# Performance work log

Hardware: AMD Instinct MI355X
Metric: run time of the kernel (lower is better)

The kernel has to match this reference:

```python
import jax, jax.numpy as jnp
import numpy as np

LOSS_WEIGHT = 0.01
CONF_THRESH = 0.8
B, N, D = 2, 12288, 256
N_CLUSTERS = 64


def setup_inputs() -> dict:
    key = jax.random.key(0)
    k1, k2, k3, k4 = jax.random.split(key, 4)
    # Clustered features so that pseudo-label confidences exceed the 0.8 threshold
    # (pure iid randn would give max cosine sim ~0.25 and a degenerate zero loss).
    centers = jax.random.normal(k1, (N_CLUSTERS, D), dtype=jnp.float32)
    ids = jax.random.randint(k2, (B, N), 0, N_CLUSTERS)
    feat_3d = centers[ids] + 0.1 * jax.random.normal(k3, (B, N, D), dtype=jnp.float32)
    valid_mask = jax.random.randint(k4, (B, N), 0, 2) == 1
    return {"feat_3d": feat_3d, "valid_mask": valid_mask}


def reference(feat_3d, valid_mask):
    # F.normalize: x / max(||x||, eps), eps=1e-12
    eps = 1e-12
    norm = jnp.sqrt(jnp.sum(feat_3d * feat_3d, axis=-1, keepdims=True))
    nf = feat_3d / jnp.maximum(norm, eps)                      # [B, N, D]

    # Full cosine-similarity matrix per scene; invalid columns masked to -inf-like.
    sim = jnp.einsum('bnd,bmd->bnm', nf, nf)                   # [B, N, N]
    neg = jnp.finfo(sim.dtype).min
    sim = jnp.where(valid_mask[:, None, :], sim, neg)
    max_sim = jnp.max(sim, axis=-1)                            # [B, N] row-max over valid cols

    invalid = ~valid_mask
    has_valid = jnp.any(valid_mask, axis=-1)                   # [B]
    has_invalid = jnp.any(invalid, axis=-1)                    # [B]

    # Only rows that are invalid points, with max similarity over valid points > threshold.
    confident = invalid & (max_sim > CONF_THRESH) & has_valid[:, None]
    n_conf = jnp.sum(confident, axis=-1)                       # [B]
    n_inv = jnp.sum(invalid, axis=-1).astype(jnp.float32)      # [B]

    contrib = jnp.where(confident, 1.0 - max_sim, 0.0)
    pseudo = jnp.sum(contrib, axis=-1) / jnp.maximum(n_conf, 1).astype(jnp.float32)

    # Scene is skipped if no valid / no invalid points or zero confident matches.
    active = (n_conf > 0) & has_valid & has_invalid
    total_loss = jnp.sum(jnp.where(active, pseudo * n_inv, 0.0))
    total_pts = jnp.sum(jnp.where(active, n_inv, 0.0))
    return jnp.where(total_pts > 0, LOSS_WEIGHT * total_loss / total_pts, 0.0)
```

## Files before the change

### kernel.cpp

```cpp
#include <hip/hip_runtime.h>

#define NTOT 12288
#define DIM  256
#define NB   2
#define BROWS 512
#define CGRP  256
#define NT    4
#define TILEB 32768
#define NGC   32
#define NRB   16

typedef __attribute__((ext_vector_type(8))) _Float16 f16x8;
typedef __attribute__((ext_vector_type(16))) float f32x16;

__device__ __forceinline__ unsigned toOrd(float f) {
    unsigned u = __float_as_uint(f);
    return (u & 0x80000000u) ? ~u : (u | 0x80000000u);
}
__device__ __forceinline__ float fromOrd(unsigned u) {
    unsigned b = (u & 0x80000000u) ? (u ^ 0x80000000u) : ~u;
    return __uint_as_float(b);
}
__device__ __forceinline__ void load_lds16(const void* g, void* l) {
    __builtin_amdgcn_global_load_lds(
        (const __attribute__((address_space(1))) unsigned int*)g,
        (__attribute__((address_space(3))) unsigned int*)l, 16, 0, 0);
}


__global__ __launch_bounds__(1024) void k_scan(
    const int* __restrict__ mask, int* __restrict__ inv,
    unsigned* __restrict__ maxsim, int* __restrict__ cnts)
{
    int b = blockIdx.x;
    int tid = threadIdx.x;
    int lane = tid & 63, w = tid >> 6;
    __shared__ int wsum[16];

    int mv[12];
    #pragma unroll
    for (int j = 0; j < 12; j++) mv[j] = mask[b * NTOT + j * 1024 + tid] ? 1 : 0;

    int running = 0;
    #pragma unroll
    for (int j = 0; j < 12; j++) {
        int i = j * 1024 + tid;
        int m = mv[j];
        int v = m;
        #pragma unroll
        for (int off = 1; off < 64; off <<= 1) {
            int t = __shfl_up(v, off);
            if (lane >= off) v += t;
        }
        if (lane == 63) wsum[w] = v;
        __syncthreads();
        int woff = 0, ctot = 0;
        #pragma unroll
        for (int k = 0; k < 16; k++) { int s = wsum[k]; ctot += s; if (k < w) woff += s; }
        int ex = running + woff + v - m;
        int d = m ? ex : (NTOT - 1 - (i - ex));
        inv[b * NTOT + d] = i;
        maxsim[b * NTOT + i] = 0u;
        running += ctot;
        __syncthreads();
    }
    if (tid == 0) { cnts[b] = running; cnts[NB + b] = NTOT - running; }
}

__global__ __launch_bounds__(256) void k_norm(
    const float* __restrict__ feat, const int* __restrict__ inv, ushort* __restrict__ pk)
{
    int blk = blockIdx.x;
    int b = blk / (NTOT / 32);
    int panel = blk % (NTOT / 32);
    int tid = threadIdx.x;
    int r = tid >> 3, c = tid & 7;
    int d = panel * 32 + r;
    int i = inv[b * NTOT + d];
    const float* src = feat + ((size_t)b * NTOT + i) * DIM + c * 32;

    float x[32]; float ss = 0.f;
    #pragma unroll
    for (int j = 0; j < 8; j++) {
        float4 v = *(const float4*)(src + j * 4);
        x[j*4+0] = v.x; x[j*4+1] = v.y; x[j*4+2] = v.z; x[j*4+3] = v.w;
        ss += v.x*v.x + v.y*v.y + v.z*v.z + v.w*v.w;
    }
    ss += __shfl_xor(ss, 1); ss += __shfl_xor(ss, 2); ss += __shfl_xor(ss, 4);
    float invn = 1.0f / fmaxf(sqrtf(ss), 1e-12f);

    ushort* pbout = pk + (size_t)b * NTOT * DIM;
    #pragma unroll
    for (int g = 0; g < 4; g++) {
        f16x8 hv;
        #pragma unroll
        for (int e = 0; e < 8; e++) hv[e] = (_Float16)(x[g*8+e] * invn);
        int kc = c * 2 + (g >> 1), kh = g & 1;
        *(f16x8*)(pbout + (size_t)(panel * 16 + kc) * 512 + (kh * 32 + r) * 8) = hv;
    }
}

__global__ __launch_bounds__(512, 2) void k_gemm(
    const ushort* __restrict__ pk, unsigned* __restrict__ maxsim, const int* __restrict__ cnts)
{
    int b = blockIdx.z;
    int nval = cnts[b];
    int ninv = cnts[NB + b];
    int bx = blockIdx.x;
    int by = blockIdx.y;
    if (bx * CGRP >= nval || by * BROWS >= ninv) return;
    int rowA0 = NTOT - (by + 1) * BROWS;
    int colG0 = bx * CGRP;
    int pA0 = rowA0 >> 5, pBg = colG0 >> 5;

    __shared__ __align__(16) char smem[4 * TILEB];

    int tid = threadIdx.x, lane = tid & 63, w = tid >> 6;
    const ushort* pb = pk + (size_t)b * NTOT * DIM;

    f16x8 a[2][16];
    {
        const ushort* abase = pb + (size_t)(pA0 + w * 2) * 16 * 512 + lane * 8;
        #pragma unroll
        for (int mt = 0; mt < 2; mt++)
            #pragma unroll
            for (int ks = 0; ks < 16; ks++)
                a[mt][ks] = *(const f16x8*)(abase + (size_t)(mt * 16 + ks) * 512);
    }
    __builtin_amdgcn_sched_barrier(0);

#define STAGE(t) { const int bo_ = ((t) & 3) * TILEB; const int p0_ = pBg + (t) * 2;     \
    _Pragma("unroll")                                                                    \
    for (int c_ = 0; c_ < 4; c_++) {                                                     \
        int c__ = w * 4 + c_;                                                            \
        const ushort* g__ = pb + ((size_t)(p0_ + (c__ >> 4)) * 16 + (c__ & 15)) * 512 + lane * 8; \
        load_lds16(g__, smem + bo_ + c__ * 1024);                                        \
    }                                                                                    \
    __builtin_amdgcn_sched_barrier(0); }

    STAGE(0); STAGE(1); STAGE(2);

    float mrow[2][16];
    #pragma unroll
    for (int mt = 0; mt < 2; mt++)
        #pragma unroll
        for (int rr = 0; rr < 16; rr++) mrow[mt][rr] = -INFINITY;

    const f32x16 zacc = {};

    #pragma unroll
    for (int t = 0; t < NT; t++) {
        if (t <= 1)      asm volatile("s_waitcnt vmcnt(8)" ::: "memory");
        else if (t == 2) asm volatile("s_waitcnt vmcnt(4)" ::: "memory");
        else             asm volatile("s_waitcnt vmcnt(0)" ::: "memory");
        __builtin_amdgcn_s_barrier();
        __builtin_amdgcn_sched_barrier(0);
        if (t + 3 < NT) STAGE(t + 3);

        const char* sb = smem + (t & 3) * TILEB;
        #pragma unroll
        for (int nt = 0; nt < 2; nt++) {
            f32x16 acc[2] = {zacc, zacc};
            #pragma unroll
            for (int kq = 0; kq < 4; kq++) {
                f16x8 bg[4];
                #pragma unroll
                for (int k4 = 0; k4 < 4; k4++)
                    bg[k4] = *(const f16x8*)(sb + (nt * 16 + kq * 4 + k4) * 1024 + lane * 16);
                #pragma unroll
                for (int k4 = 0; k4 < 4; k4++)
                    #pragma unroll
                    for (int mt = 0; mt < 2; mt++)
                        acc[mt] = __builtin_amdgcn_mfma_f32_32x32x16_f16(
                            a[mt][kq * 4 + k4], bg[k4], acc[mt], 0, 0, 0);
            }
            int cg = colG0 + t * 64 + nt * 32 + (lane & 31);
            bool cv = cg < nval;
            #pragma unroll
            for (int mt = 0; mt < 2; mt++)
                #pragma unroll
                for (int rr = 0; rr < 16; rr++) {
                    float vv = cv ? acc[mt][rr] : -INFINITY;
                    mrow[mt][rr] = fmaxf(mrow[mt][rr], vv);
                }
        }
    }
#undef STAGE

    #pragma unroll
    for (int off = 1; off <= 16; off <<= 1)
        #pragma unroll
        for (int mt = 0; mt < 2; mt++)
            #pragma unroll
            for (int rr = 0; rr < 16; rr++)
                mrow[mt][rr] = fmaxf(mrow[mt][rr], __shfl_xor(mrow[mt][rr], off));

    int cl = lane & 31, hh = lane >> 5;
    if (cl == 0) {
        #pragma unroll
        for (int mt = 0; mt < 2; mt++)
            #pragma unroll
            for (int rr = 0; rr < 16; rr++) {
                int rowg = rowA0 + w * 64 + mt * 32 + (rr & 3) + 8 * (rr >> 2) + 4 * hh;
                atomicMax(maxsim + (size_t)b * NTOT + rowg, toOrd(mrow[mt][rr]));
            }
    }
}

__global__ __launch_bounds__(256) void k_final(
    const unsigned* __restrict__ maxsim, const int* __restrict__ cnts, float* __restrict__ out)
{
    __shared__ float ssum[NB];
    __shared__ int   scnt[NB];
    int tid = threadIdx.x;
    if (tid < NB) { ssum[tid] = 0.0f; scnt[tid] = 0; }
    __syncthreads();

    for (int b = 0; b < NB; b++) {
        int ninv = cnts[NB + b];
        float ls = 0.0f; int lc = 0;
        for (int i = tid; i < ninv; i += 256) {
            int r = NTOT - ninv + i;
            float ms = fromOrd(maxsim[(size_t)b * NTOT + r]);
            if (ms > 0.8f) { ls += 1.0f - ms; lc++; }
        }
        #pragma unroll
        for (int off = 32; off; off >>= 1) {
            ls += __shfl_xor(ls, off);
            lc += __shfl_xor(lc, off);
        }
        if ((tid & 63) == 0) { atomicAdd(&ssum[b], ls); atomicAdd(&scnt[b], lc); }
    }
    __syncthreads();

    if (tid == 0) {
        float tl = 0.0f, tp = 0.0f;
        for (int b = 0; b < NB; b++) {
            int nval = cnts[b], ninv = cnts[NB + b], nc = scnt[b];
            bool active = (nc > 0) && (nval > 0) && (ninv > 0);
            if (active) {
                float pseudo = ssum[b] / (float)(nc > 0 ? nc : 1);
                tl += pseudo * (float)ninv;
                tp += (float)ninv;
            }
        }
        out[0] = (tp > 0.0f) ? (0.01f * tl / tp) : 0.0f;
    }
}

extern "C" void kernel_launch(void* const* d_in, const int* in_sizes, int n_in,
                              void* d_out, int out_size, void* d_ws, size_t ws_size,
                              hipStream_t stream)
{
    const float* feat = (const float*)d_in[0];
    const int*   mask = (const int*)d_in[1];

    char* ws = (char*)d_ws;
    int*      cnts   = (int*)ws;
    int*      inv    = (int*)(ws + 64);
    unsigned* maxsim = (unsigned*)(ws + 98368);
    ushort*   pk     = (ushort*)(ws + 262144);

    hipLaunchKernelGGL(k_scan, dim3(NB), dim3(1024), 0, stream, mask, inv, maxsim, cnts);
    hipLaunchKernelGGL(k_norm, dim3(NB * (NTOT / 32)), dim3(256), 0, stream, feat, inv, pk);
    hipLaunchKernelGGL(k_gemm, dim3(NGC, NRB, NB), dim3(512), 0, stream, pk, maxsim, cnts);
    hipLaunchKernelGGL(k_final, dim3(1), dim3(256), 0, stream, maxsim, cnts, (float*)d_out);
}
```

Before: 159.3 us.

## Split GEMM block work across 16 waves with one M-tile per wave

Doubles the GEMM block to 1024 threads. Each wave now holds a single 32-row A tile instead of two, which halves the A registers and accumulators per wave and lets more waves be resident. Cooperative LDS staging is spread over twice as many waves, the vmcnt waits are adjusted to match, and s_setprio is placed around the MFMA bursts. The final reduction also uses 1024 threads. The trade-off is less MFMA work per B fragment read from LDS, so LDS read traffic per FLOP doubles.

```diff
diff --git a/kernel.cpp b/kernel.cpp
--- a/kernel.cpp
+++ b/kernel.cpp
@@ -100,7 +100,7 @@
     }
 }
 
-__global__ __launch_bounds__(512, 2) void k_gemm(
+__global__ __launch_bounds__(1024, 4) void k_gemm(
     const ushort* __restrict__ pk, unsigned* __restrict__ maxsim, const int* __restrict__ cnts)
 {
     int b = blockIdx.z;
@@ -118,21 +118,19 @@
     int tid = threadIdx.x, lane = tid & 63, w = tid >> 6;
     const ushort* pb = pk + (size_t)b * NTOT * DIM;
 
-    f16x8 a[2][16];
+    f16x8 a[16];
     {
-        const ushort* abase = pb + (size_t)(pA0 + w * 2) * 16 * 512 + lane * 8;
-        #pragma unroll
-        for (int mt = 0; mt < 2; mt++)
-            #pragma unroll
-            for (int ks = 0; ks < 16; ks++)
-                a[mt][ks] = *(const f16x8*)(abase + (size_t)(mt * 16 + ks) * 512);
+        const ushort* abase = pb + (size_t)(pA0 + w) * 16 * 512 + lane * 8;
+        #pragma unroll
+        for (int ks = 0; ks < 16; ks++)
+            a[ks] = *(const f16x8*)(abase + (size_t)ks * 512);
     }
     __builtin_amdgcn_sched_barrier(0);
 
 #define STAGE(t) { const int bo_ = ((t) & 3) * TILEB; const int p0_ = pBg + (t) * 2;     \
     _Pragma("unroll")                                                                    \
-    for (int c_ = 0; c_ < 4; c_++) {                                                     \
-        int c__ = w * 4 + c_;                                                            \
+    for (int c_ = 0; c_ < 2; c_++) {                                                     \
+        int c__ = w * 2 + c_;                                                            \
         const ushort* g__ = pb + ((size_t)(p0_ + (c__ >> 4)) * 16 + (c__ & 15)) * 512 + lane * 8; \
         load_lds16(g__, smem + bo_ + c__ * 1024);                                        \
     }                                                                                    \
@@ -140,18 +138,16 @@
 
     STAGE(0); STAGE(1); STAGE(2);
 
-    float mrow[2][16];
-    #pragma unroll
-    for (int mt = 0; mt < 2; mt++)
-        #pragma unroll
-        for (int rr = 0; rr < 16; rr++) mrow[mt][rr] = -INFINITY;
+    float mrow[16];
+    #pragma unroll
+    for (int rr = 0; rr < 16; rr++) mrow[rr] = -INFINITY;
 
     const f32x16 zacc = {};
 
     #pragma unroll
     for (int t = 0; t < NT; t++) {
-        if (t <= 1)      asm volatile("s_waitcnt vmcnt(8)" ::: "memory");
-        else if (t == 2) asm volatile("s_waitcnt vmcnt(4)" ::: "memory");
+        if (t <= 1)      asm volatile("s_waitcnt vmcnt(4)" ::: "memory");
+        else if (t == 2) asm volatile("s_waitcnt vmcnt(2)" ::: "memory");
         else             asm volatile("s_waitcnt vmcnt(0)" ::: "memory");
         __builtin_amdgcn_s_barrier();
         __builtin_amdgcn_sched_barrier(0);
@@ -160,29 +156,27 @@
         const char* sb = smem + (t & 3) * TILEB;
         #pragma unroll
         for (int nt = 0; nt < 2; nt++) {
-            f32x16 acc[2] = {zacc, zacc};
+            f32x16 acc = zacc;
             #pragma unroll
             for (int kq = 0; kq < 4; kq++) {
                 f16x8 bg[4];
                 #pragma unroll
                 for (int k4 = 0; k4 < 4; k4++)
                     bg[k4] = *(const f16x8*)(sb + (nt * 16 + kq * 4 + k4) * 1024 + lane * 16);
+                __builtin_amdgcn_s_setprio(1);
                 #pragma unroll
                 for (int k4 = 0; k4 < 4; k4++)
-                    #pragma unroll
-                    for (int mt = 0; mt < 2; mt++)
-                        acc[mt] = __builtin_amdgcn_mfma_f32_32x32x16_f16(
-                            a[mt][kq * 4 + k4], bg[k4], acc[mt], 0, 0, 0);
+                    acc = __builtin_amdgcn_mfma_f32_32x32x16_f16(
+                        a[kq * 4 + k4], bg[k4], acc, 0, 0, 0);
+                __builtin_amdgcn_s_setprio(0);
             }
             int cg = colG0 + t * 64 + nt * 32 + (lane & 31);
             bool cv = cg < nval;
             #pragma unroll
-            for (int mt = 0; mt < 2; mt++)
-                #pragma unroll
-                for (int rr = 0; rr < 16; rr++) {
-                    float vv = cv ? acc[mt][rr] : -INFINITY;
-                    mrow[mt][rr] = fmaxf(mrow[mt][rr], vv);
-                }
+            for (int rr = 0; rr < 16; rr++) {
+                float vv = cv ? acc[rr] : -INFINITY;
+                mrow[rr] = fmaxf(mrow[rr], vv);
+            }
         }
     }
 #undef STAGE
@@ -190,24 +184,20 @@
     #pragma unroll
     for (int off = 1; off <= 16; off <<= 1)
         #pragma unroll
-        for (int mt = 0; mt < 2; mt++)
-            #pragma unroll
-            for (int rr = 0; rr < 16; rr++)
-                mrow[mt][rr] = fmaxf(mrow[mt][rr], __shfl_xor(mrow[mt][rr], off));
+        for (int rr = 0; rr < 16; rr++)
+            mrow[rr] = fmaxf(mrow[rr], __shfl_xor(mrow[rr], off));
 
     int cl = lane & 31, hh = lane >> 5;
     if (cl == 0) {
         #pragma unroll
-        for (int mt = 0; mt < 2; mt++)
-            #pragma unroll
-            for (int rr = 0; rr < 16; rr++) {
-                int rowg = rowA0 + w * 64 + mt * 32 + (rr & 3) + 8 * (rr >> 2) + 4 * hh;
-                atomicMax(maxsim + (size_t)b * NTOT + rowg, toOrd(mrow[mt][rr]));
-            }
-    }
-}
-
-__global__ __launch_bounds__(256) void k_final(
+        for (int rr = 0; rr < 16; rr++) {
+            int rowg = rowA0 + w * 32 + (rr & 3) + 8 * (rr >> 2) + 4 * hh;
+            atomicMax(maxsim + (size_t)b * NTOT + rowg, toOrd(mrow[rr]));
+        }
+    }
+}
+
+__global__ __launch_bounds__(1024) void k_final(
     const unsigned* __restrict__ maxsim, const int* __restrict__ cnts, float* __restrict__ out)
 {
     __shared__ float ssum[NB];
@@ -219,7 +209,7 @@
     for (int b = 0; b < NB; b++) {
         int ninv = cnts[NB + b];
         float ls = 0.0f; int lc = 0;
-        for (int i = tid; i < ninv; i += 256) {
+        for (int i = tid; i < ninv; i += 1024) {
             int r = NTOT - ninv + i;
             float ms = fromOrd(maxsim[(size_t)b * NTOT + r]);
             if (ms > 0.8f) { ls += 1.0f - ms; lc++; }
@@ -263,6 +253,6 @@
 
     hipLaunchKernelGGL(k_scan, dim3(NB), dim3(1024), 0, stream, mask, inv, maxsim, cnts);
     hipLaunchKernelGGL(k_norm, dim3(NB * (NTOT / 32)), dim3(256), 0, stream, feat, inv, pk);
-    hipLaunchKernelGGL(k_gemm, dim3(NGC, NRB, NB), dim3(512), 0, stream, pk, maxsim, cnts);
-    hipLaunchKernelGGL(k_final, dim3(1), dim3(256), 0, stream, maxsim, cnts, (float*)d_out);
-}
+    hipLaunchKernelGGL(k_gemm, dim3(NGC, NRB, NB), dim3(1024), 0, stream, pk, maxsim, cnts);
+    hipLaunchKernelGGL(k_final, dim3(1), dim3(1024), 0, stream, maxsim, cnts, (float*)d_out);
+}
```

Result: no change. 158.3 us (-0.6%).

## Fuse final reduction into GEMM via last-block counter and retile GEMM grid

Applied to the files above, without the earlier changes.

Removes the separate k_final launch: each GEMM block bumps a global counter after its atomics, and the last block to finish runs the loss reduction. The GEMM moves to 256-thread blocks with 256-row tiles, a 26x26 grid sized to cover the valid and invalid halves more tightly, double buffering instead of four stages, and s_setprio around the MFMA bursts. k_norm now stages each packed panel in LDS so the global writes are coalesced. The risks are more blocks with less A-reuse per block, and a grid-wide counter whose correctness relies on the fence ordering.

```diff
diff --git a/kernel.cpp b/kernel.cpp
--- a/kernel.cpp
+++ b/kernel.cpp
@@ -3,12 +3,13 @@
 #define NTOT 12288
 #define DIM  256
 #define NB   2
-#define BROWS 512
+#define BROWS 256
 #define CGRP  256
 #define NT    4
 #define TILEB 32768
-#define NGC   32
-#define NRB   16
+#define NGC   26
+#define NRB   26
+#define GRID_TOT (NGC * NRB * NB)
 
 typedef __attribute__((ext_vector_type(8))) _Float16 f16x8;
 typedef __attribute__((ext_vector_type(16))) float f32x16;
@@ -36,6 +37,8 @@
     int tid = threadIdx.x;
     int lane = tid & 63, w = tid >> 6;
     __shared__ int wsum[16];
+
+    if (b == 0 && tid == 0) ((unsigned*)cnts)[4] = 0u;
 
     int mv[12];
     #pragma unroll
@@ -70,13 +73,13 @@
 __global__ __launch_bounds__(256) void k_norm(
     const float* __restrict__ feat, const int* __restrict__ inv, ushort* __restrict__ pk)
 {
+    __shared__ __align__(16) ushort pan[16][512];
     int blk = blockIdx.x;
     int b = blk / (NTOT / 32);
     int panel = blk % (NTOT / 32);
     int tid = threadIdx.x;
     int r = tid >> 3, c = tid & 7;
-    int d = panel * 32 + r;
-    int i = inv[b * NTOT + d];
+    int i = inv[b * NTOT + panel * 32 + r];
     const float* src = feat + ((size_t)b * NTOT + i) * DIM + c * 32;
 
     float x[32]; float ss = 0.f;
@@ -89,162 +92,171 @@
     ss += __shfl_xor(ss, 1); ss += __shfl_xor(ss, 2); ss += __shfl_xor(ss, 4);
     float invn = 1.0f / fmaxf(sqrtf(ss), 1e-12f);
 
-    ushort* pbout = pk + (size_t)b * NTOT * DIM;
     #pragma unroll
     for (int g = 0; g < 4; g++) {
         f16x8 hv;
         #pragma unroll
         for (int e = 0; e < 8; e++) hv[e] = (_Float16)(x[g*8+e] * invn);
         int kc = c * 2 + (g >> 1), kh = g & 1;
-        *(f16x8*)(pbout + (size_t)(panel * 16 + kc) * 512 + (kh * 32 + r) * 8) = hv;
-    }
-}
-
-__global__ __launch_bounds__(512, 2) void k_gemm(
-    const ushort* __restrict__ pk, unsigned* __restrict__ maxsim, const int* __restrict__ cnts)
-{
+        *(f16x8*)&pan[kc][(kh * 32 + r) * 8] = hv;
+    }
+    __syncthreads();
+
+    f16x8* dst = (f16x8*)(pk + (size_t)b * NTOT * DIM + (size_t)panel * 16 * 512);
+    const f16x8* srcl = (const f16x8*)pan;
+    #pragma unroll
+    for (int j = 0; j < 4; j++) dst[tid + j * 256] = srcl[tid + j * 256];
+}
+
+__global__ __launch_bounds__(256, 2) void k_gemm(
+    const ushort* __restrict__ pk, unsigned* __restrict__ maxsim,
+    int* __restrict__ cnts, float* __restrict__ out)
+{
+    __shared__ __align__(16) char smem[2 * TILEB];
+
     int b = blockIdx.z;
     int nval = cnts[b];
     int ninv = cnts[NB + b];
     int bx = blockIdx.x;
     int by = blockIdx.y;
-    if (bx * CGRP >= nval || by * BROWS >= ninv) return;
-    int rowA0 = NTOT - (by + 1) * BROWS;
-    int colG0 = bx * CGRP;
-    int pA0 = rowA0 >> 5, pBg = colG0 >> 5;
-
-    __shared__ __align__(16) char smem[4 * TILEB];
-
     int tid = threadIdx.x, lane = tid & 63, w = tid >> 6;
-    const ushort* pb = pk + (size_t)b * NTOT * DIM;
-
-    f16x8 a[2][16];
-    {
-        const ushort* abase = pb + (size_t)(pA0 + w * 2) * 16 * 512 + lane * 8;
+    unsigned* donecnt = (unsigned*)cnts + 4;
+
+    bool active = (bx * CGRP < nval) && (by * BROWS < ninv);
+    if (active) {
+        int rowA0 = NTOT - (by + 1) * BROWS;
+        int colG0 = bx * CGRP;
+        int pA0 = rowA0 >> 5, pBg = colG0 >> 5;
+        const ushort* pb = pk + (size_t)b * NTOT * DIM;
+
+        f16x8 a[2][16];
+        {
+            const ushort* abase = pb + (size_t)(pA0 + w * 2) * 16 * 512 + lane * 8;
+            #pragma unroll
+            for (int mt = 0; mt < 2; mt++)
+                #pragma unroll
+                for (int ks = 0; ks < 16; ks++)
+                    a[mt][ks] = *(const f16x8*)(abase + (size_t)(mt * 16 + ks) * 512);
+        }
+        __builtin_amdgcn_sched_barrier(0);
+
+#define STAGE(t) { const int bo_ = ((t) & 1) * TILEB; const int p0_ = pBg + (t) * 2;  \
+    _Pragma("unroll")                                                                 \
+    for (int c_ = 0; c_ < 8; c_++) {                                                  \
+        int c__ = w * 8 + c_;                                                         \
+        const ushort* g__ = pb + ((size_t)(p0_ + (c__ >> 4)) * 16 + (c__ & 15)) * 512 + lane * 8; \
+        load_lds16(g__, smem + bo_ + c__ * 1024);                                     \
+    }                                                                                 \
+    __builtin_amdgcn_sched_barrier(0); }
+
+        STAGE(0); STAGE(1);
+
+        float mrow[2][16];
         #pragma unroll
         for (int mt = 0; mt < 2; mt++)
             #pragma unroll
-            for (int ks = 0; ks < 16; ks++)
-                a[mt][ks] = *(const f16x8*)(abase + (size_t)(mt * 16 + ks) * 512);
-    }
-    __builtin_amdgcn_sched_barrier(0);
-
-#define STAGE(t) { const int bo_ = ((t) & 3) * TILEB; const int p0_ = pBg + (t) * 2;     \
-    _Pragma("unroll")                                                                    \
-    for (int c_ = 0; c_ < 4; c_++) {                                                     \
-        int c__ = w * 4 + c_;                                                            \
-        const ushort* g__ = pb + ((size_t)(p0_ + (c__ >> 4)) * 16 + (c__ & 15)) * 512 + lane * 8; \
-        load_lds16(g__, smem + bo_ + c__ * 1024);                                        \
-    }                                                                                    \
-    __builtin_amdgcn_sched_barrier(0); }
-
-    STAGE(0); STAGE(1); STAGE(2);
-
-    float mrow[2][16];
-    #pragma unroll
-    for (int mt = 0; mt < 2; mt++)
-        #pragma unroll
-        for (int rr = 0; rr < 16; rr++) mrow[mt][rr] = -INFINITY;
-
-    const f32x16 zacc = {};
-
-    #pragma unroll
-    for (int t = 0; t < NT; t++) {
-        if (t <= 1)      asm volatile("s_waitcnt vmcnt(8)" ::: "memory");
-        else if (t == 2) asm volatile("s_waitcnt vmcnt(4)" ::: "memory");
-        else             asm volatile("s_waitcnt vmcnt(0)" ::: "memory");
-        __builtin_amdgcn_s_barrier();
-        __builtin_amdgcn_sched_barrier(0);
-        if (t + 3 < NT) STAGE(t + 3);
-
-        const char* sb = smem + (t & 3) * TILEB;
-        #pragma unroll
-        for (int nt = 0; nt < 2; nt++) {
-            f32x16 acc[2] = {zacc, zacc};
-            #pragma unroll
-            for (int kq = 0; kq < 4; kq++) {
-                f16x8 bg[4];
-                #pragma unroll
-                for (int k4 = 0; k4 < 4; k4++)
-                    bg[k4] = *(const f16x8*)(sb + (nt * 16 + kq * 4 + k4) * 1024 + lane * 16);
-                #pragma unroll
-                for (int k4 = 0; k4 < 4; k4++)
+            for (int rr = 0; rr < 16; rr++) mrow[mt][rr] = -INFINITY;
+
+        const f32x16 zacc = {};
+
+        #pragma unroll
+        for (int t = 0; t < NT; t++) {
+            if (t < NT - 1) asm volatile("s_waitcnt vmcnt(8)" ::: "memory");
+            else            asm volatile("s_waitcnt vmcnt(0)" ::: "memory");
+            __builtin_amdgcn_s_barrier();
+            __builtin_amdgcn_sched_barrier(0);
+
+            const char* sb = smem + (t & 1) * TILEB;
+            #pragma unroll
+            for (int nt = 0; nt < 2; nt++) {
+                f32x16 acc0 = zacc, acc1 = zacc;
+                #pragma unroll
+                for (int kq = 0; kq < 4; kq++) {
+                    f16x8 bg[4];
                     #pragma unroll
-                    for (int mt = 0; mt < 2; mt++)
-                        acc[mt] = __builtin_amdgcn_mfma_f32_32x32x16_f16(
-                            a[mt][kq * 4 + k4], bg[k4], acc[mt], 0, 0, 0);
-            }
-            int cg = colG0 + t * 64 + nt * 32 + (lane & 31);
-            bool cv = cg < nval;
+                    for (int k4 = 0; k4 < 4; k4++)
+                        bg[k4] = *(const f16x8*)(sb + (nt * 16 + kq * 4 + k4) * 1024 + lane * 16);
+                    __builtin_amdgcn_s_setprio(1);
+                    #pragma unroll
+                    for (int k4 = 0; k4 < 4; k4++) {
+                        acc0 = __builtin_amdgcn_mfma_f32_32x32x16_f16(a[0][kq*4+k4], bg[k4], acc0, 0, 0, 0);
+                        acc1 = __builtin_amdgcn_mfma_f32_32x32x16_f16(a[1][kq*4+k4], bg[k4], acc1, 0, 0, 0);
+                    }
+                    __builtin_amdgcn_s_setprio(0);
+                }
+                int cg = colG0 + t * 64 + nt * 32 + (lane & 31);
+                bool cv = cg < nval;
+                #pragma unroll
+                for (int rr = 0; rr < 16; rr++) {
+                    mrow[0][rr] = fmaxf(mrow[0][rr], cv ? acc0[rr] : -INFINITY);
+                    mrow[1][rr] = fmaxf(mrow[1][rr], cv ? acc1[rr] : -INFINITY);
+                }
+            }
+            __builtin_amdgcn_s_barrier();
+            if (t + 2 < NT) STAGE(t + 2);
+        }
+#undef STAGE
+
+        #pragma unroll
+        for (int off = 1; off <= 16; off <<= 1)
             #pragma unroll
             for (int mt = 0; mt < 2; mt++)
                 #pragma unroll
+                for (int rr = 0; rr < 16; rr++)
+                    mrow[mt][rr] = fmaxf(mrow[mt][rr], __shfl_xor(mrow[mt][rr], off));
+
+        int cl = lane & 31, hh = lane >> 5;
+        if (cl == 0) {
+            #pragma unroll
+            for (int mt = 0; mt < 2; mt++)
+                #pragma unroll
                 for (int rr = 0; rr < 16; rr++) {
-                    float vv = cv ? acc[mt][rr] : -INFINITY;
-                    mrow[mt][rr] = fmaxf(mrow[mt][rr], vv);
-                }
-        }
-    }
-#undef STAGE
-
-    #pragma unroll
-    for (int off = 1; off <= 16; off <<= 1)
-        #pragma unroll
-        for (int mt = 0; mt < 2; mt++)
-            #pragma unroll
-            for (int rr = 0; rr < 16; rr++)
-                mrow[mt][rr] = fmaxf(mrow[mt][rr], __shfl_xor(mrow[mt][rr], off));
-
-    int cl = lane & 31, hh = lane >> 5;
-    if (cl == 0) {
-        #pragma unroll
-        for (int mt = 0; mt < 2; mt++)
-            #pragma unroll
-            for (int rr = 0; rr < 16; rr++) {
-                int rowg = rowA0 + w * 64 + mt * 32 + (rr & 3) + 8 * (rr >> 2) + 4 * hh;
-                atomicMax(maxsim + (size_t)b * NTOT + rowg, toOrd(mrow[mt][rr]));
-            }
-    }
-}
-
-__global__ __launch_bounds__(256) void k_final(
-    const unsigned* __restrict__ maxsim, const int* __restrict__ cnts, float* __restrict__ out)
-{
-    __shared__ float ssum[NB];
-    __shared__ int   scnt[NB];
-    int tid = threadIdx.x;
-    if (tid < NB) { ssum[tid] = 0.0f; scnt[tid] = 0; }
+                    int rowg = rowA0 + w * 64 + mt * 32 + (rr & 3) + 8 * (rr >> 2) + 4 * hh;
+                    atomicMax(maxsim + (size_t)b * NTOT + rowg, toOrd(mrow[mt][rr]));
+                }
+        }
+    }
+
+    __threadfence();
     __syncthreads();
-
-    for (int b = 0; b < NB; b++) {
-        int ninv = cnts[NB + b];
-        float ls = 0.0f; int lc = 0;
-        for (int i = tid; i < ninv; i += 256) {
-            int r = NTOT - ninv + i;
-            float ms = fromOrd(maxsim[(size_t)b * NTOT + r]);
-            if (ms > 0.8f) { ls += 1.0f - ms; lc++; }
-        }
-        #pragma unroll
-        for (int off = 32; off; off >>= 1) {
-            ls += __shfl_xor(ls, off);
-            lc += __shfl_xor(lc, off);
-        }
-        if ((tid & 63) == 0) { atomicAdd(&ssum[b], ls); atomicAdd(&scnt[b], lc); }
-    }
+    unsigned* sflag = (unsigned*)smem;
+    if (tid == 0) *sflag = atomicAdd(donecnt, 1u);
     __syncthreads();
-
-    if (tid == 0) {
-        float tl = 0.0f, tp = 0.0f;
-        for (int b = 0; b < NB; b++) {
-            int nval = cnts[b], ninv = cnts[NB + b], nc = scnt[b];
-            bool active = (nc > 0) && (nval > 0) && (ninv > 0);
-            if (active) {
-                float pseudo = ssum[b] / (float)(nc > 0 ? nc : 1);
-                tl += pseudo * (float)ninv;
-                tp += (float)ninv;
-            }
-        }
-        out[0] = (tp > 0.0f) ? (0.01f * tl / tp) : 0.0f;
+    if (*sflag == GRID_TOT - 1) {
+        __threadfence();
+        float* ssum = (float*)(smem + 16);
+        int*   scnt = (int*)(smem + 32);
+        if (tid < NB) { ssum[tid] = 0.0f; scnt[tid] = 0; }
+        __syncthreads();
+        for (int bb = 0; bb < NB; bb++) {
+            int ninv2 = cnts[NB + bb];
+            float ls = 0.0f; int lc = 0;
+            for (int i = tid; i < ninv2; i += 256) {
+                int r = NTOT - ninv2 + i;
+                float ms = fromOrd(maxsim[(size_t)bb * NTOT + r]);
+                if (ms > 0.8f) { ls += 1.0f - ms; lc++; }
+            }
+            #pragma unroll
+            for (int off = 32; off; off >>= 1) {
+                ls += __shfl_xor(ls, off);
+                lc += __shfl_xor(lc, off);
+            }
+            if ((tid & 63) == 0) { atomicAdd(&ssum[bb], ls); atomicAdd(&scnt[bb], lc); }
+        }
+        __syncthreads();
+        if (tid == 0) {
+            float tl = 0.0f, tp = 0.0f;
+            for (int bb = 0; bb < NB; bb++) {
+                int nval2 = cnts[bb], ninv2 = cnts[NB + bb], nc = scnt[bb];
+                bool act = (nc > 0) && (nval2 > 0) && (ninv2 > 0);
+                if (act) {
+                    float pseudo = ssum[bb] / (float)(nc > 0 ? nc : 1);
+                    tl += pseudo * (float)ninv2;
+                    tp += (float)ninv2;
+                }
+            }
+            out[0] = (tp > 0.0f) ? (0.01f * tl / tp) : 0.0f;
+        }
     }
 }
 
@@ -263,6 +275,6 @@
 
     hipLaunchKernelGGL(k_scan, dim3(NB), dim3(1024), 0, stream, mask, inv, maxsim, cnts);
     hipLaunchKernelGGL(k_norm, dim3(NB * (NTOT / 32)), dim3(256), 0, stream, feat, inv, pk);
-    hipLaunchKernelGGL(k_gemm, dim3(NGC, NRB, NB), dim3(512), 0, stream, pk, maxsim, cnts);
-    hipLaunchKernelGGL(k_final, dim3(1), dim3(256), 0, stream, maxsim, cnts, (float*)d_out);
-}
+    hipLaunchKernelGGL(k_gemm, dim3(NGC, NRB, NB), dim3(256), 0, stream,
+                       pk, maxsim, cnts, (float*)d_out);
+}
```

New measurement: 278.6 us. 1.75x slower.
